# Performance work log

Measured on AMD Instinct MI355X. Metric: run time of the kernel, lower is better.

Reference implementation:

```python
import jax, jax.numpy as jnp
import numpy as np

EPS = 1e-4  # Coqui LayerNorm (type '1') eps


def _layer_norm_c(x, g, b):
    # x: (B, C, T); normalize over channel dim 1 (Coqui LayerNorm type '1')
    m = jnp.mean(x, axis=1, keepdims=True)
    v = jnp.var(x, axis=1, keepdims=True)
    return (x - m) * jax.lax.rsqrt(v + EPS) * g[None, :, None] + b[None, :, None]


def _s4d(x, log_dt, A_re, A_im, C_re, C_im, D, Wout, bout):
    # S4 (mode='diag' / S4D) layer, transposed=True -> x: (B, H, L)
    L = x.shape[-1]
    dt = jnp.exp(log_dt)[:, None]                       # (H, 1)
    A = A_re + 1j * A_im                                # (H, N2) diagonal SSM
    dtA = A * dt                                        # (H, N2)
    Cd = (C_re + 1j * C_im) * (jnp.exp(dtA) - 1.0) / A  # ZOH-discretized C (B absorbed)
    vand = jnp.exp(dtA[:, :, None] * jnp.arange(L))     # (H, N2, L) Vandermonde
    K = 2.0 * jnp.einsum('hn,hnl->hl', Cd, vand).real   # (H, L) SSM conv kernel
    n = 2 * L                                           # causal conv via FFT
    y = jnp.fft.irfft(jnp.fft.rfft(x, n=n) * jnp.fft.rfft(K, n=n)[None], n=n)[..., :L]
    y = y + D[None, :, None] * x                        # skip connection
    y = jax.nn.gelu(y, approximate=False)               # dropout=0 (eval)
    z = jnp.einsum('oh,bhl->bol', Wout, y) + bout[None, :, None]  # (B, 2H, L)
    a, g = jnp.split(z, 2, axis=1)                      # GLU over channel dim
    return a * jax.nn.sigmoid(g)


def _ffn(x, x_mask, W1, b1, W2, b2):
    # kernel_size=1 feed-forward conv block with masking
    h = jnp.einsum('fh,bhl->bfl', W1, x * x_mask) + b1[None, :, None]
    h = jax.nn.relu(h)
    o = jnp.einsum('of,bfl->bol', W2, h * x_mask) + b2[None, :, None]
    return o * x_mask


def reference(x, x_mask, log_dt, A_re, A_im, C_re, C_im, D, Wout, bout,
              g1, be1, W1, bf1, W2, bf2, g2, be2):
    n_layers = log_dt.shape[0]
    for i in range(n_layers):
        x = x * x_mask
        y = _s4d(x, log_dt[i], A_re[i], A_im[i], C_re[i], C_im[i],
                 D[i], Wout[i], bout[i])
        x = _layer_norm_c(x + y, g1[i], be1[i])
        y = _ffn(x, x_mask, W1[i], bf1[i], W2[i], bf2[i])
        x = _layer_norm_c(x + y, g2[i], be2[i])
    return x * x_mask


def setup_inputs():
    Lyr, B, H, T, N2, HF = 6, 16, 384, 2048, 32, 1536
    key = jax.random.key(0)
    ks = jax.random.split(key, 8)
    x = jax.random.normal(ks[0], (B, H, T), jnp.float32)
    x_mask = jnp.ones((B, 1, T), jnp.float32)
    # stable S4D init: log_dt in [log 1e-3, log 1e-1], A = -1/2 + i*pi*n
    log_dt = (jax.random.uniform(ks[1], (Lyr, H), jnp.float32)
              * (np.log(0.1) - np.log(0.001)) + np.log(0.001))
    A_re = -0.5 * jnp.ones((Lyr, H, N2), jnp.float32)
    A_im = jnp.broadcast_to(np.pi * jnp.arange(N2, dtype=np.float32),
                            (Lyr, H, N2)) * jnp.ones((1,), jnp.float32)
    C_re = jax.random.normal(ks[2], (Lyr, H, N2), jnp.float32) * 0.5 ** 0.5
    C_im = jax.random.normal(ks[3], (Lyr, H, N2), jnp.float32) * 0.5 ** 0.5
    D = jax.random.normal(ks[4], (Lyr, H), jnp.float32)
    Wout = jax.random.normal(ks[5], (Lyr, 2 * H, H), jnp.float32) / np.sqrt(H)
    bout = jnp.zeros((Lyr, 2 * H), jnp.float32)
    g1 = jnp.ones((Lyr, H), jnp.float32)
    be1 = jnp.zeros((Lyr, H), jnp.float32)
    W1 = jax.random.normal(ks[6], (Lyr, HF, H), jnp.float32) / np.sqrt(H)
    bf1 = jnp.zeros((Lyr, HF), jnp.float32)
    W2 = jax.random.normal(ks[7], (Lyr, H, HF), jnp.float32) / np.sqrt(HF)
    bf2 = jnp.zeros((Lyr, H), jnp.float32)
    g2 = jnp.ones((Lyr, H), jnp.float32)
    be2 = jnp.zeros((Lyr, H), jnp.float32)
    return {"x": x, "x_mask": x_mask, "log_dt": log_dt, "A_re": A_re,
            "A_im": A_im, "C_re": C_re, "C_im": C_im, "D": D,
            "Wout": Wout, "bout": bout, "g1": g1, "be1": be1,
            "W1": W1, "bf1": bf1, "W2": W2, "bf2": bf2,
            "g2": g2, "be2": be2}
```

## Files before the change

kernel.cpp:

```cpp
#include <hip/hip_runtime.h>
#include <math.h>

#define Bq 16
#define Hc 384
#define Tt 2048
#define N2 32
#define LYR 6
#define HFq 1536
#define TWOH 768
#define CHUNK 64
#define NCH (Tt/CHUNK)
#define NJ (Bq*NCH)
#define UH (NJ*CHUNK)

typedef __bf16 bf16x8 __attribute__((ext_vector_type(8)));
typedef float floatx4 __attribute__((ext_vector_type(4)));
typedef _Float16 f16_t;
typedef f16_t fp16x8 __attribute__((ext_vector_type(8)));
typedef f16_t fp16x4 __attribute__((ext_vector_type(4)));

__device__ __forceinline__ unsigned short bfbits(float f) {
  union { float f; unsigned u; } x; x.f = f;
  return (unsigned short)((x.u + 0x7FFF + ((x.u >> 16) & 1)) >> 16);
}
__device__ __forceinline__ float bf2f(unsigned short u) {
  union { unsigned u; float f; } x; x.u = ((unsigned)u) << 16; return x.f;
}

__global__ void param_kernel(const float* __restrict__ log_dt,
                             const float* __restrict__ A_re, const float* __restrict__ A_im,
                             const float* __restrict__ C_re, const float* __restrict__ C_im,
                             float* __restrict__ wre, float* __restrict__ wim,
                             float* __restrict__ cdre, float* __restrict__ cdim,
                             float* __restrict__ wSre, float* __restrict__ wSim) {
  int idx = blockIdx.x * blockDim.x + threadIdx.x;
  if (idx >= LYR * Hc * N2) return;
  int hn = idx / N2;
  double dt = exp((double)log_dt[hn]);
  double are = (double)A_re[idx], aim = (double)A_im[idx];
  double dre = are * dt, dimv = aim * dt;
  double er = exp(dre);
  double wr = er * cos(dimv), wi_ = er * sin(dimv);
  double den = are * are + aim * aim;
  double nr = wr - 1.0, ni = wi_;
  double qr = (nr * are + ni * aim) / den;
  double qi = (ni * are - nr * aim) / den;
  double cr = (double)C_re[idx], ci = (double)C_im[idx];
  cdre[idx] = (float)(2.0 * (cr * qr - ci * qi));
  cdim[idx] = (float)(2.0 * (cr * qi + ci * qr));
  wre[idx] = (float)wr; wim[idx] = (float)wi_;
  double es = exp(dre * (double)CHUNK);
  wSre[idx] = (float)(es * cos(dimv * (double)CHUNK));
  wSim[idx] = (float)(es * sin(dimv * (double)CHUNK));
}

__global__ void cvt_bf16_kernel(const float* __restrict__ in, unsigned short* __restrict__ out,
                                int n4) {
  int idx = blockIdx.x * 256 + threadIdx.x;
  if (idx >= n4) return;
  float4 v = ((const float4*)in)[idx];
  ushort4 o;
  o.x = bfbits(v.x); o.y = bfbits(v.y); o.z = bfbits(v.z); o.w = bfbits(v.w);
  ((ushort4*)out)[idx] = o;
}

__global__ __launch_bounds__(256) void transpose_fwd(const float* __restrict__ in,
                                                     float* __restrict__ out) {
  __shared__ float tile[32][33];
  int tx = threadIdx.x, ty = threadIdx.y;
  int t0 = blockIdx.x * 32, c0 = blockIdx.y * 32, b = blockIdx.z;
#pragma unroll
  for (int k = 0; k < 4; k++)
    tile[ty + 8 * k][tx] = in[((size_t)(b * Hc + c0 + ty + 8 * k)) * Tt + t0 + tx];
  __syncthreads();
#pragma unroll
  for (int k = 0; k < 4; k++)
    out[((size_t)(b * Tt + t0 + ty + 8 * k)) * Hc + c0 + tx] = tile[tx][ty + 8 * k];
}

__global__ __launch_bounds__(256) void transpose_bwd(const float* __restrict__ in,
                                                     const float* __restrict__ mask,
                                                     float* __restrict__ out) {
  __shared__ float tile[32][33];
  int tx = threadIdx.x, ty = threadIdx.y;
  int t0 = blockIdx.x * 32, c0 = blockIdx.y * 32, b = blockIdx.z;
#pragma unroll
  for (int k = 0; k < 4; k++)
    tile[ty + 8 * k][tx] = in[((size_t)(b * Tt + t0 + ty + 8 * k)) * Hc + c0 + tx];
  __syncthreads();
  float mv = mask[(size_t)b * Tt + t0 + tx];
#pragma unroll
  for (int k = 0; k < 4; k++)
    out[((size_t)(b * Hc + c0 + ty + 8 * k)) * Tt + t0 + tx] = tile[tx][ty + 8 * k] * mv;
}

__global__ __launch_bounds__(256) void pack_u(const float* __restrict__ xT,
                                              const float* __restrict__ mask,
                                              f16_t* __restrict__ U) {
  __shared__ float tile[64][65];
  int tid = threadIdx.x;
  int t0 = blockIdx.x * 64, h0 = blockIdx.y * 64, b = blockIdx.z;
#pragma unroll
  for (int p = 0; p < 4; p++) {
    int idx = p * 256 + tid;
    int row = idx >> 4, c4 = (idx & 15) * 4;
    float4 v = *(const float4*)&xT[((size_t)(b * Tt + t0 + row)) * Hc + h0 + c4];
    float mv = mask[(size_t)b * Tt + t0 + row];
    tile[row][c4] = v.x * mv; tile[row][c4 + 1] = v.y * mv;
    tile[row][c4 + 2] = v.z * mv; tile[row][c4 + 3] = v.w * mv;
  }
  __syncthreads();
#pragma unroll
  for (int p = 0; p < 2; p++) {
    int idx = p * 256 + tid;
    int hr = idx >> 3, g = (idx & 7) * 8;
    fp16x8 o;
#pragma unroll
    for (int i = 0; i < 8; i++) o[i] = (f16_t)tile[g + i][hr];
    *(fp16x8*)&U[(size_t)(h0 + hr) * UH + (size_t)b * Tt + t0 + g] = o;
  }
}

__global__ __launch_bounds__(256) void build_mats(
    const float* __restrict__ wre, const float* __restrict__ wim,
    const float* __restrict__ cdre, const float* __restrict__ cdim,
    f16_t* __restrict__ Ag, f16_t* __restrict__ Wg) {
  __shared__ float pre[65][32], pim[65][32], Kc[64], cdr_s[32], cdi_s[32];
  int h = blockIdx.x, tid = threadIdx.x;
  if (tid < 32) {
    float wr = wre[h * N2 + tid], wi = wim[h * N2 + tid];
    cdr_s[tid] = cdre[h * N2 + tid];
    cdi_s[tid] = cdim[h * N2 + tid];
    float pr = 1.f, pi = 0.f;
    for (int p = 0; p <= 64; p++) {
      pre[p][tid] = pr; pim[p][tid] = pi;
      float nr2 = pr * wr - pi * wi;
      pi = pr * wi + pi * wr;
      pr = nr2;
    }
  }
  __syncthreads();
  if (tid < 64) {
    float s = 0.f;
    for (int n = 0; n < 32; n++)
      s = fmaf(cdr_s[n], pre[tid][n], fmaf(-cdi_s[n], pim[tid][n], s));
    Kc[tid] = s;
  }
  __syncthreads();
  for (int i = tid; i < 64 * 128; i += 256) {
    int m = i >> 7, k = i & 127;
    float v;
    if (k < 64) {
      v = (m >= k) ? Kc[m - k] : 0.f;
    } else {
      int kk = k - 64, n = kk >> 1;
      v = (kk & 1) ? -fmaf(cdr_s[n], pim[m + 1][n], cdi_s[n] * pre[m + 1][n])
                   :  fmaf(cdr_s[n], pre[m + 1][n], -cdi_s[n] * pim[m + 1][n]);
    }
    Ag[(size_t)h * 8192 + i] = (f16_t)v;
  }
  for (int i = tid; i < 64 * 64; i += 256) {
    int m = i >> 6, tau = i & 63, n = m >> 1;
    float v = (m & 1) ? pim[63 - tau][n] : pre[63 - tau][n];
    Wg[(size_t)h * 4096 + i] = (f16_t)v;
  }
}

__global__ __launch_bounds__(256) void gemm_state(const f16_t* __restrict__ U,
                                                  const f16_t* __restrict__ Wg,
                                                  f16_t* __restrict__ St) {
  __shared__ f16_t Aw[64][72];
  __shared__ f16_t Bu[128][72];
  int tid = threadIdx.x;
  int j0 = blockIdx.x * 128, h = blockIdx.y;
#pragma unroll
  for (int p = 0; p < 2; p++) {
    int idx = p * 256 + tid;
    int row = idx >> 3, c8 = (idx & 7) * 8;
    *(fp16x8*)&Aw[row][c8] = *(const fp16x8*)&Wg[(size_t)h * 4096 + row * 64 + c8];
  }
#pragma unroll
  for (int p = 0; p < 4; p++) {
    int idx = p * 256 + tid;
    int row = idx >> 3, c8 = (idx & 7) * 8;
    *(fp16x8*)&Bu[row][c8] =
        *(const fp16x8*)&U[(size_t)h * UH + (size_t)(j0 + row) * CHUNK + c8];
  }
  __syncthreads();
  int wave = tid >> 6, lane = tid & 63, l16 = lane & 15, quad = lane >> 4;
  int m0 = wave * 16;
  floatx4 acc[8];
#pragma unroll
  for (int jt = 0; jt < 8; jt++) acc[jt] = (floatx4){0.f, 0.f, 0.f, 0.f};
#pragma unroll
  for (int kk = 0; kk < 2; kk++) {
    fp16x8 a = *(const fp16x8*)&Aw[m0 + l16][kk * 32 + quad * 8];
#pragma unroll
    for (int jt = 0; jt < 8; jt++) {
      fp16x8 bb = *(const fp16x8*)&Bu[jt * 16 + l16][kk * 32 + quad * 8];
      acc[jt] = __builtin_amdgcn_mfma_f32_16x16x32_f16(a, bb, acc[jt], 0, 0, 0);
    }
  }
#pragma unroll
  for (int jt = 0; jt < 8; jt++) {
    int j = j0 + jt * 16 + l16;
    fp16x4 o;
#pragma unroll
    for (int r = 0; r < 4; r++) o[r] = (f16_t)acc[jt][r];
    *(fp16x4*)&St[(size_t)h * UH + (size_t)j * CHUNK + m0 + quad * 4] = o;
  }
}

__global__ __launch_bounds__(256) void scan_prefix2(
    f16_t* __restrict__ St,
    const float* __restrict__ wSre, const float* __restrict__ wSim) {
  int gid = blockIdx.x * 256 + threadIdx.x;
  if (gid >= Hc * Bq * N2) return;
  int n = gid & 31;
  int b = (gid >> 5) & 15;
  int h = gid >> 9;
  float wr = wSre[h * N2 + n], wi = wSim[h * N2 + n];
  float cr = 0.f, ci = 0.f;
  unsigned* base = (unsigned*)(St + (size_t)h * UH + (size_t)b * Tt + 2 * n);
  for (int c = 0; c < NCH; c++) {
    union { unsigned u; f16_t h2[2]; } in, out;
    in.u = base[c * 32];
    float sre = (float)in.h2[0], sim = (float)in.h2[1];
    out.h2[0] = (f16_t)cr; out.h2[1] = (f16_t)ci;
    base[c * 32] = out.u;
    float c0 = cr;
    cr = fmaf(wr, c0, fmaf(-wi, ci, sre));
    ci = fmaf(wr, ci, fmaf(wi, c0, sim));
  }
}

__global__ __launch_bounds__(256) void gemm_out(
    const f16_t* __restrict__ U, const f16_t* __restrict__ Ag,
    const f16_t* __restrict__ St, const float* __restrict__ Dv,
    unsigned short* __restrict__ Yb) {
  __shared__ f16_t Aa[64][136];
  __shared__ f16_t Bb[128][136];
  int tid = threadIdx.x;
  int j0 = blockIdx.x * 128, h = blockIdx.y;
#pragma unroll
  for (int p = 0; p < 4; p++) {
    int idx = p * 256 + tid;
    int row = idx >> 4, c8 = (idx & 15) * 8;
    *(fp16x8*)&Aa[row][c8] = *(const fp16x8*)&Ag[(size_t)h * 8192 + row * 128 + c8];
  }
#pragma unroll
  for (int p = 0; p < 4; p++) {
    int idx = p * 256 + tid;
    int row = idx >> 3, c8 = (idx & 7) * 8;
    *(fp16x8*)&Bb[row][c8] =
        *(const fp16x8*)&U[(size_t)h * UH + (size_t)(j0 + row) * CHUNK + c8];
    *(fp16x8*)&Bb[row][64 + c8] =
        *(const fp16x8*)&St[(size_t)h * UH + (size_t)(j0 + row) * CHUNK + c8];
  }
  __syncthreads();
  int wave = tid >> 6, lane = tid & 63, l16 = lane & 15, quad = lane >> 4;
  int m0 = wave * 16;
  floatx4 acc[8];
#pragma unroll
  for (int jt = 0; jt < 8; jt++) acc[jt] = (floatx4){0.f, 0.f, 0.f, 0.f};
#pragma unroll
  for (int kk = 0; kk < 4; kk++) {
    fp16x8 a = *(const fp16x8*)&Aa[m0 + l16][kk * 32 + quad * 8];
#pragma unroll
    for (int jt = 0; jt < 8; jt++) {
      fp16x8 bb = *(const fp16x8*)&Bb[jt * 16 + l16][kk * 32 + quad * 8];
      acc[jt] = __builtin_amdgcn_mfma_f32_16x16x32_f16(a, bb, acc[jt], 0, 0, 0);
    }
  }
  float d = Dv[h];
  int tb = m0 + quad * 4;
#pragma unroll
  for (int jt = 0; jt < 8; jt++) {
    int jr = jt * 16 + l16;
    fp16x4 u4 = *(const fp16x4*)&Bb[jr][tb];
    ushort4 o;
#pragma unroll
    for (int r = 0; r < 4; r++) {
      float v = fmaf(d, (float)u4[r], acc[jt][r]);
      v = 0.5f * v * (1.0f + erff(v * 0.70710678118654752f));
      ((unsigned short*)&o)[r] = bfbits(v);
    }
    *(ushort4*)&Yb[(size_t)h * UH + (size_t)(j0 + jr) * CHUNK + tb] = o;
  }
}

__global__ __launch_bounds__(256) void unpack_y(const unsigned short* __restrict__ Yb,
                                                unsigned short* __restrict__ yb) {
  __shared__ unsigned short tile[64][65];
  int tid = threadIdx.x;
  int t0 = blockIdx.x * 64, h0 = blockIdx.y * 64, b = blockIdx.z;
#pragma unroll
  for (int p = 0; p < 2; p++) {
    int idx = p * 256 + tid;
    int hr = idx >> 3, g = (idx & 7) * 8;
    uint4 v = *(const uint4*)&Yb[(size_t)(h0 + hr) * UH + (size_t)b * Tt + t0 + g];
    const unsigned short* s = (const unsigned short*)&v;
#pragma unroll
    for (int i = 0; i < 8; i++) tile[hr][g + i] = s[i];
  }
  __syncthreads();
#pragma unroll
  for (int p = 0; p < 2; p++) {
    int idx = p * 256 + tid;
    int tr = idx >> 3, g = (idx & 7) * 8;
    unsigned short o[8];
#pragma unroll
    for (int i = 0; i < 8; i++) o[i] = tile[g + i][tr];
    *(uint4*)&yb[((size_t)(b * Tt + t0 + tr)) * Hc + h0 + g] = *(uint4*)o;
  }
}

template <int EPI>
__global__ __launch_bounds__(256) void mfma_gemm(
    const __bf16* __restrict__ act, const __bf16* __restrict__ W,
    const float* __restrict__ bias, const float* __restrict__ mask,
    unsigned short* __restrict__ outb, int K, int NOUT) {
  __shared__ __bf16 As[128][32];
  __shared__ __bf16 Bs[128][32];
  __shared__ __bf16 Bs2[(EPI == 2) ? 128 : 1][32];
  int tid = threadIdx.x;
  int b = blockIdx.z;
  int t0 = blockIdx.x * 128, n0 = blockIdx.y * 128;
  int wave = tid >> 6, lane = tid & 63, l16 = lane & 15, quad = lane >> 4;
  int wm = wave >> 1, wn = wave & 1;
  int sr = tid >> 2, sk = (tid & 3) * 8;

  floatx4 acc[4][4];
  floatx4 accg[(EPI == 2) ? 4 : 1][4];
#pragma unroll
  for (int i = 0; i < 4; i++)
#pragma unroll
    for (int j = 0; j < 4; j++) {
      acc[i][j] = (floatx4){0.f, 0.f, 0.f, 0.f};
      if constexpr (EPI == 2) accg[i][j] = (floatx4){0.f, 0.f, 0.f, 0.f};
    }

  const __bf16* aPtr = act + ((size_t)(b * Tt + t0 + sr)) * K + sk;
  const __bf16* bPtr = W + (size_t)(n0 + sr) * K + sk;
  const __bf16* gPtr = (EPI == 2) ? (W + (size_t)(NOUT + n0 + sr) * K + sk) : bPtr;

  for (int k0 = 0; k0 < K; k0 += 32) {
    uint4 a0 = *(const uint4*)(aPtr + k0);
    uint4 a1 = *(const uint4*)(aPtr + k0 + (size_t)64 * K);
    uint4 w0 = *(const uint4*)(bPtr + k0);
    uint4 w1 = *(const uint4*)(bPtr + k0 + (size_t)64 * K);
    uint4 g0, g1;
    if constexpr (EPI == 2) {
      g0 = *(const uint4*)(gPtr + k0);
      g1 = *(const uint4*)(gPtr + k0 + (size_t)64 * K);
    }
    __syncthreads();
    *(uint4*)&As[sr][sk] = a0; *(uint4*)&As[sr + 64][sk] = a1;
    *(uint4*)&Bs[sr][sk] = w0; *(uint4*)&Bs[sr + 64][sk] = w1;
    if constexpr (EPI == 2) { *(uint4*)&Bs2[sr][sk] = g0; *(uint4*)&Bs2[sr + 64][sk] = g1; }
    __syncthreads();
    bf16x8 af[4], bfr[4], gfr[(EPI == 2) ? 4 : 1];
#pragma unroll
    for (int i = 0; i < 4; i++)
      af[i] = *(const bf16x8*)&As[wm * 64 + i * 16 + l16][quad * 8];
#pragma unroll
    for (int j = 0; j < 4; j++) {
      bfr[j] = *(const bf16x8*)&Bs[wn * 64 + j * 16 + l16][quad * 8];
      if constexpr (EPI == 2)
        gfr[j] = *(const bf16x8*)&Bs2[wn * 64 + j * 16 + l16][quad * 8];
    }
#pragma unroll
    for (int i = 0; i < 4; i++)
#pragma unroll
      for (int j = 0; j < 4; j++) {
        acc[i][j] = __builtin_amdgcn_mfma_f32_16x16x32_bf16(af[i], bfr[j], acc[i][j], 0, 0, 0);
        if constexpr (EPI == 2)
          accg[i][j] = __builtin_amdgcn_mfma_f32_16x16x32_bf16(af[i], gfr[j], accg[i][j], 0, 0, 0);
      }
  }

#pragma unroll
  for (int i = 0; i < 4; i++) {
    int tb = t0 + wm * 64 + i * 16 + quad * 4;
    float mv[4];
    if constexpr (EPI == 1) {
#pragma unroll
      for (int r = 0; r < 4; r++) mv[r] = mask[(size_t)b * Tt + tb + r];
    }
#pragma unroll
    for (int j = 0; j < 4; j++) {
      int n = n0 + wn * 64 + j * 16 + l16;
      float bn = bias[n];
      float bg = (EPI == 2) ? bias[NOUT + n] : 0.f;
#pragma unroll
      for (int r = 0; r < 4; r++) {
        size_t o = ((size_t)(b * Tt + tb + r)) * NOUT + n;
        if constexpr (EPI == 0) {
          outb[o] = bfbits(acc[i][j][r] + bn);
        } else if constexpr (EPI == 1) {
          float v = fmaxf(acc[i][j][r] + bn, 0.f) * mv[r];
          outb[o] = bfbits(v);
        } else {
          float a = acc[i][j][r] + bn;
          float g = accg[i][j][r] + bg;
          outb[o] = bfbits(a / (1.f + expf(-g)));
        }
      }
    }
  }
}

__global__ __launch_bounds__(256) void ln_t(
    const float* __restrict__ in1, const unsigned short* __restrict__ in2b,
    const float* __restrict__ mask, const float* __restrict__ gamma,
    const float* __restrict__ beta, float* __restrict__ out,
    unsigned short* __restrict__ outb, int m1, int m2) {
  int row = blockIdx.x * 4 + (threadIdx.x >> 6);
  int lane = threadIdx.x & 63;
  float mv = mask[row];
  float f1 = m1 ? mv : 1.f;
  float f2 = m2 ? mv : 1.f;
  size_t base = (size_t)row * Hc;
  float v[6], sum = 0.f, sq = 0.f;
#pragma unroll
  for (int j = 0; j < 6; j++) {
    int idx = lane + 64 * j;
    float a = in1[base + idx] * f1 + bf2f(in2b[base + idx]) * f2;
    v[j] = a; sum += a; sq = fmaf(a, a, sq);
  }
#pragma unroll
  for (int off = 32; off >= 1; off >>= 1) {
    sum += __shfl_xor(sum, off, 64);
    sq  += __shfl_xor(sq,  off, 64);
  }
  float m = sum * (1.f / Hc);
  float var = sq * (1.f / Hc) - m * m;
  float rs = rsqrtf(var + 1e-4f);
#pragma unroll
  for (int j = 0; j < 6; j++) {
    int idx = lane + 64 * j;
    float o = (v[j] - m) * rs * gamma[idx] + beta[idx];
    out[base + idx] = o;
    if (outb) outb[base + idx] = bfbits(o * mv);
  }
}

__global__ void diag_kernel(float* out, float v) {
  if (blockIdx.x == 0 && threadIdx.x == 0) out[0] = v;
}

extern "C" void kernel_launch(void* const* d_in, const int* in_sizes, int n_in,
                              void* d_out, int out_size, void* d_ws, size_t ws_size,
                              hipStream_t stream) {
  const float* x_in  = (const float*)d_in[0];
  const float* xmask = (const float*)d_in[1];
  const float* log_dt = (const float*)d_in[2];
  const float* A_re = (const float*)d_in[3];
  const float* A_im = (const float*)d_in[4];
  const float* C_re = (const float*)d_in[5];
  const float* C_im = (const float*)d_in[6];
  const float* Dv   = (const float*)d_in[7];
  const float* Wout = (const float*)d_in[8];
  const float* bout = (const float*)d_in[9];
  const float* g1   = (const float*)d_in[10];
  const float* be1  = (const float*)d_in[11];
  const float* W1   = (const float*)d_in[12];
  const float* bf1  = (const float*)d_in[13];
  const float* W2   = (const float*)d_in[14];
  const float* bf2  = (const float*)d_in[15];
  const float* g2   = (const float*)d_in[16];
  const float* be2  = (const float*)d_in[17];

  const size_t NXf   = (size_t)Bq * Hc * Tt;
  const size_t NP    = (size_t)LYR * Hc * N2;
  const size_t YBFf  = NXf / 2;
  const size_t HBFf  = (size_t)Bq * Tt * HFq / 2;
  const size_t WOUTf = (size_t)LYR * TWOH * Hc / 2;
  const size_t W1f   = (size_t)LYR * HFq * Hc / 2;
  const size_t W2f   = (size_t)LYR * Hc * HFq / 2;

  size_t need = 2 * NXf + YBFf + HBFf + WOUTf + W1f + W2f + 6 * NP;
  if (ws_size / 4 < need) {
    diag_kernel<<<1, 64, 0, stream>>>((float*)d_out, 1000.0f + (float)(ws_size >> 20));
    return;
  }

  float* ws = (float*)d_ws;
  float* xT   = ws;
  float* tmp  = xT + NXf;
  float* ybfF = tmp + NXf;
  float* hbfF = ybfF + YBFf;
  float* wobF = hbfF + HBFf;
  float* w1bF = wobF + WOUTf;
  float* w2bF = w1bF + W1f;
  float* wre  = w2bF + W2f;
  float* wim  = wre + NP;
  float* cdre = wim + NP;
  float* cdim = cdre + NP;
  float* wSre = cdim + NP;
  float* wSim = wSre + NP;

  unsigned short* ybf = (unsigned short*)ybfF;
  unsigned short* hbf = (unsigned short*)hbfF;
  unsigned short* wob = (unsigned short*)wobF;
  unsigned short* w1b = (unsigned short*)w1bF;
  unsigned short* w2b = (unsigned short*)w2bF;
  float* x1 = (float*)d_out;

  f16_t* Ub   = (f16_t*)tmp;
  unsigned short* tmpb = (unsigned short*)(tmp + NXf / 2);
  f16_t* St16 = (f16_t*)hbfF;
  unsigned short* Ybi = (unsigned short*)(hbfF + YBFf);
  f16_t* Ag   = (f16_t*)(hbfF + 2 * YBFf);
  f16_t* Wg   = Ag + (size_t)384 * 8192;

  param_kernel<<<(LYR * Hc * N2 + 255) / 256, 256, 0, stream>>>(
      log_dt, A_re, A_im, C_re, C_im, wre, wim, cdre, cdim, wSre, wSim);
  cvt_bf16_kernel<<<(int)(2 * WOUTf + 1023) / 1024, 256, 0, stream>>>(Wout, wob, (int)(WOUTf / 2));
  cvt_bf16_kernel<<<(int)(2 * W1f + 1023) / 1024, 256, 0, stream>>>(W1, w1b, (int)(W1f / 2));
  cvt_bf16_kernel<<<(int)(2 * W2f + 1023) / 1024, 256, 0, stream>>>(W2, w2b, (int)(W2f / 2));
  transpose_fwd<<<dim3(Tt / 32, Hc / 32, Bq), dim3(32, 8), 0, stream>>>(x_in, xT);

  for (int i = 0; i < LYR; i++) {
    size_t po = (size_t)i * Hc * N2;

    pack_u<<<dim3(Tt / 64, Hc / 64, Bq), 256, 0, stream>>>(xT, xmask, Ub);
    build_mats<<<Hc, 256, 0, stream>>>(wre + po, wim + po, cdre + po, cdim + po, Ag, Wg);
    gemm_state<<<dim3(NJ / 128, Hc), 256, 0, stream>>>(Ub, Wg, St16);
    scan_prefix2<<<(Hc * Bq * N2) / 256, 256, 0, stream>>>(St16, wSre + po, wSim + po);
    gemm_out<<<dim3(NJ / 128, Hc), 256, 0, stream>>>(Ub, Ag, St16, Dv + (size_t)i * Hc, Ybi);
    unpack_y<<<dim3(Tt / 64, Hc / 64, Bq), 256, 0, stream>>>(Ybi, ybf);

    mfma_gemm<2><<<dim3(Tt / 128, Hc / 128, Bq), 256, 0, stream>>>(
        (const __bf16*)ybf, (const __bf16*)(wob + (size_t)i * TWOH * Hc),
        bout + (size_t)i * TWOH, xmask, tmpb, Hc, Hc);

    ln_t<<<(Bq * Tt) / 4, 256, 0, stream>>>(
        xT, tmpb, xmask, g1 + (size_t)i * Hc, be1 + (size_t)i * Hc, x1, ybf, 1, 0);

    mfma_gemm<1><<<dim3(Tt / 128, HFq / 128, Bq), 256, 0, stream>>>(
        (const __bf16*)ybf, (const __bf16*)(w1b + (size_t)i * HFq * Hc),
        bf1 + (size_t)i * HFq, xmask, hbf, Hc, HFq);

    mfma_gemm<0><<<dim3(Tt / 128, Hc / 128, Bq), 256, 0, stream>>>(
        (const __bf16*)hbf, (const __bf16*)(w2b + (size_t)i * Hc * HFq),
        bf2 + (size_t)i * Hc, xmask, tmpb, HFq, Hc);

    ln_t<<<(Bq * Tt) / 4, 256, 0, stream>>>(
        x1, tmpb, xmask, g2 + (size_t)i * Hc, be2 + (size_t)i * Hc, xT, nullptr, 0, 1);
  }

  transpose_bwd<<<dim3(Tt / 32, Hc / 32, Bq), dim3(32, 8), 0, stream>>>(xT, xmask, (float*)d_out);
}
```

Baseline: 1.988 ms.

## Double-buffer GEMM tiles with direct global-to-LDS async loads

Replaces the register-staged global-load-then-LDS-store path in the MFMA GEMM with global_load_lds direct transfers into LDS, and adds a second LDS buffer. The next K-slice is prefetched while the current one feeds the MFMAs, so there is one barrier per iteration instead of two. This targets load latency and register pressure in the main GEMM loop, at the cost of doubled LDS use, which may lower occupancy. It relies on the wave-uniform LDS base semantics of the builtin and on correct vmcnt waits before the barrier.

```diff
diff --git a/kernel.cpp b/kernel.cpp
--- a/kernel.cpp
+++ b/kernel.cpp
@@ -25,6 +25,12 @@
 }
 __device__ __forceinline__ float bf2f(unsigned short u) {
   union { unsigned u; float f; } x; x.u = ((unsigned)u) << 16; return x.f;
+}
+
+__device__ __forceinline__ void gl_lds16(const void* g, void* l) {
+  __builtin_amdgcn_global_load_lds(
+      (const __attribute__((address_space(1))) void*)g,
+      (__attribute__((address_space(3))) void*)l, 16, 0, 0);
 }
 
 __global__ void param_kernel(const float* __restrict__ log_dt,
@@ -320,15 +326,14 @@
     const __bf16* __restrict__ act, const __bf16* __restrict__ W,
     const float* __restrict__ bias, const float* __restrict__ mask,
     unsigned short* __restrict__ outb, int K, int NOUT) {
-  __shared__ __bf16 As[128][32];
-  __shared__ __bf16 Bs[128][32];
-  __shared__ __bf16 Bs2[(EPI == 2) ? 128 : 1][32];
+  __shared__ __bf16 As[2][128][32];
+  __shared__ __bf16 Bs[2][128][32];
+  __shared__ __bf16 Bs2[(EPI == 2) ? 2 : 1][(EPI == 2) ? 128 : 1][32];
   int tid = threadIdx.x;
   int b = blockIdx.z;
   int t0 = blockIdx.x * 128, n0 = blockIdx.y * 128;
   int wave = tid >> 6, lane = tid & 63, l16 = lane & 15, quad = lane >> 4;
   int wm = wave >> 1, wn = wave & 1;
-  int sr = tid >> 2, sk = (tid & 3) * 8;
 
   floatx4 acc[4][4];
   floatx4 accg[(EPI == 2) ? 4 : 1][4];
@@ -340,34 +345,36 @@
       if constexpr (EPI == 2) accg[i][j] = (floatx4){0.f, 0.f, 0.f, 0.f};
     }
 
-  const __bf16* aPtr = act + ((size_t)(b * Tt + t0 + sr)) * K + sk;
-  const __bf16* bPtr = W + (size_t)(n0 + sr) * K + sk;
-  const __bf16* gPtr = (EPI == 2) ? (W + (size_t)(NOUT + n0 + sr) * K + sk) : bPtr;
-
+  int srow = wave * 16 + (lane >> 2);
+  int scol = (lane & 3) * 8;
+  const __bf16* aSrc = act + ((size_t)(b * Tt + t0 + srow)) * K + scol;
+  const __bf16* bSrc = W + (size_t)(n0 + srow) * K + scol;
+  const __bf16* gSrc = W + (size_t)(NOUT + n0 + srow) * K + scol;
+
+  auto stage = [&](int buf, int k0) {
+#pragma unroll
+    for (int r = 0; r < 2; r++) {
+      gl_lds16(aSrc + k0 + (size_t)(64 * r) * K, &As[buf][wave * 16 + r * 64][0]);
+      gl_lds16(bSrc + k0 + (size_t)(64 * r) * K, &Bs[buf][wave * 16 + r * 64][0]);
+      if constexpr (EPI == 2)
+        gl_lds16(gSrc + k0 + (size_t)(64 * r) * K, &Bs2[buf][wave * 16 + r * 64][0]);
+    }
+  };
+
+  stage(0, 0);
+  __syncthreads();
+  int cur = 0;
   for (int k0 = 0; k0 < K; k0 += 32) {
-    uint4 a0 = *(const uint4*)(aPtr + k0);
-    uint4 a1 = *(const uint4*)(aPtr + k0 + (size_t)64 * K);
-    uint4 w0 = *(const uint4*)(bPtr + k0);
-    uint4 w1 = *(const uint4*)(bPtr + k0 + (size_t)64 * K);
-    uint4 g0, g1;
-    if constexpr (EPI == 2) {
-      g0 = *(const uint4*)(gPtr + k0);
-      g1 = *(const uint4*)(gPtr + k0 + (size_t)64 * K);
-    }
-    __syncthreads();
-    *(uint4*)&As[sr][sk] = a0; *(uint4*)&As[sr + 64][sk] = a1;
-    *(uint4*)&Bs[sr][sk] = w0; *(uint4*)&Bs[sr + 64][sk] = w1;
-    if constexpr (EPI == 2) { *(uint4*)&Bs2[sr][sk] = g0; *(uint4*)&Bs2[sr + 64][sk] = g1; }
-    __syncthreads();
+    if (k0 + 32 < K) stage(cur ^ 1, k0 + 32);
     bf16x8 af[4], bfr[4], gfr[(EPI == 2) ? 4 : 1];
 #pragma unroll
     for (int i = 0; i < 4; i++)
-      af[i] = *(const bf16x8*)&As[wm * 64 + i * 16 + l16][quad * 8];
+      af[i] = *(const bf16x8*)&As[cur][wm * 64 + i * 16 + l16][quad * 8];
 #pragma unroll
     for (int j = 0; j < 4; j++) {
-      bfr[j] = *(const bf16x8*)&Bs[wn * 64 + j * 16 + l16][quad * 8];
+      bfr[j] = *(const bf16x8*)&Bs[cur][wn * 64 + j * 16 + l16][quad * 8];
       if constexpr (EPI == 2)
-        gfr[j] = *(const bf16x8*)&Bs2[wn * 64 + j * 16 + l16][quad * 8];
+        gfr[j] = *(const bf16x8*)&Bs2[cur][wn * 64 + j * 16 + l16][quad * 8];
     }
 #pragma unroll
     for (int i = 0; i < 4; i++)
@@ -377,6 +384,8 @@
         if constexpr (EPI == 2)
           accg[i][j] = __builtin_amdgcn_mfma_f32_16x16x32_bf16(af[i], gfr[j], accg[i][j], 0, 0, 0);
       }
+    __syncthreads();
+    cur ^= 1;
   }
 
 #pragma unroll
```

After: 1.901 ms. 1.05x faster.
